# Kernel tuning notes

Measured on AMD Instinct MI355X. Metric: run time of the kernel, lower is better.

## Reference

```python
import jax, jax.numpy as jnp
import numpy as np

B, T = 64, 500
NUM_CONCEPT, DIM, SIZE_MEM = 1024, 64, 50


def setup_inputs() -> dict:
    key = jax.random.key(0)
    ks = jax.random.split(key, 16)
    d = DIM

    def lin(k, fin, fout):
        k1, k2 = jax.random.split(k)
        s = 1.0 / np.sqrt(fin)
        return (jax.random.uniform(k1, (fin, fout), jnp.float32, -s, s),
                jax.random.uniform(k2, (fout,), jnp.float32, -s, s))

    Wf, bf = lin(ks[4], 2 * d, d)
    We, be = lin(ks[5], d, d)
    Wa, ba = lin(ks[6], d, d)
    Wab, bab = lin(ks[7], d, 1)
    Wd, bd = lin(ks[8], d, 1)
    return {
        'concept_seq': jax.random.randint(ks[0], (B, T), 0, NUM_CONCEPT),
        'correct_seq': jax.random.randint(ks[1], (B, T), 0, 2),
        'num_concept': NUM_CONCEPT,
        'embed_key': jax.random.normal(ks[2], (NUM_CONCEPT, d), jnp.float32),
        'embed_value': jax.random.normal(ks[3], (2 * NUM_CONCEPT, d), jnp.float32),
        'Mk': jax.random.normal(ks[9], (SIZE_MEM, d), jnp.float32) * np.sqrt(2.0 / d),
        'Mv0': jax.random.normal(ks[10], (SIZE_MEM, d), jnp.float32) * np.sqrt(2.0 / d),
        'Wf': Wf, 'bf': bf, 'We': We, 'be': be, 'Wa': Wa, 'ba': ba,
        'Wab': Wab, 'bab': bab, 'Wd': Wd, 'bd': bd,
    }


def _forward(concept_seq, correct_seq, num_concept, embed_key, embed_value,
             Mk, Mv0, Wf, bf, We, be, Wa, ba, Wab, bab, Wd, bd):
    x = concept_seq + num_concept * correct_seq          # [B,T]
    k = embed_key[concept_seq]                           # [B,T,d]
    v = embed_value[x]                                   # [B,T,d]
    w = jax.nn.softmax(jnp.einsum('btd,sd->bts', k, Mk), axis=-1)  # [B,T,S]
    e = jax.nn.sigmoid(v @ We + be)                      # [B,T,d]
    a = jnp.tanh(v @ Wa + ba)                            # [B,T,d]

    bsz = concept_seq.shape[0]
    Mv_init = jnp.broadcast_to(Mv0, (bsz,) + Mv0.shape)  # [B,S,d]

    def step(Mvt, inp):
        wt, et, at = inp                                 # [B,S],[B,d],[B,d]
        u = wt[:, :, None]
        Mv_new = Mvt * (1.0 - u * et[:, None, :]) + u * at[:, None, :]
        return Mv_new, Mvt                               # emit pre-update state

    wT = jnp.swapaxes(w, 0, 1)                           # [T,B,S]
    eT = jnp.swapaxes(e, 0, 1)
    aT = jnp.swapaxes(a, 0, 1)
    _, Mv_pre = jax.lax.scan(step, Mv_init, (wT, eT, aT))  # [T,B,S,d]

    r = jnp.einsum('tbs,tbsd->btd', wT, Mv_pre)          # read content [B,T,d]
    f = jnp.tanh(jnp.concatenate([r, k], axis=-1) @ Wf + bf)
    stu_ability = jnp.tanh(f @ Wab + bab)                # [B,T,1] (dropout = eval identity)
    que_diff = jnp.tanh(k @ Wd + bd)                     # [B,T,1]
    return jax.nn.sigmoid(3.0 * stu_ability - que_diff)[..., 0]  # [B,T]


def reference(concept_seq, correct_seq, num_concept, embed_key, embed_value,
              Mk, Mv0, Wf, bf, We, be, Wa, ba, Wab, bab, Wd, bd):
    return _forward(concept_seq, correct_seq, num_concept, embed_key, embed_value,
                    Mk, Mv0, Wf, bf, We, be, Wa, ba, Wab, bab, Wd, bd)
```

## Files before the change

### kernel.cpp

```cpp
#include <hip/hip_runtime.h>
#include <hip/hip_bf16.h>
#include <math.h>

#define BB 64
#define TT 500
#define DD 64
#define SS 50
#define CH 20
#define NCH (TT / CH)

__device__ __forceinline__ float sigmoidf_(float x) { return 1.0f / (1.0f + __expf(-x)); }

__device__ __forceinline__ float rdlane(float v, int l) {
    return __int_as_float(__builtin_amdgcn_readlane(__float_as_int(v), l));
}

#define PIN() asm volatile("" ::: "memory")

__global__ __launch_bounds__(64) void k1_tables(
    const float* __restrict__ embed_key,
    const float* __restrict__ embed_value,
    const float* __restrict__ Mk,
    const float* __restrict__ We, const float* __restrict__ be,
    const float* __restrict__ Wa, const float* __restrict__ ba,
    int ncon, int nv,
    float* __restrict__ wTab, float* __restrict__ eaTab)
{
    const int lane = threadIdx.x;
    if ((int)blockIdx.x < ncon) {
        const int c = blockIdx.x;
        __shared__ float mkS[SS][DD + 1];
        __shared__ float kS[DD];
        kS[lane] = embed_key[c * DD + lane];
        for (int s = 0; s < SS; ++s)
            mkS[s][lane] = Mk[s * DD + lane];
        __syncthreads();

        float sc = -1e30f;
        if (lane < SS) {
            float acc = 0.f;
            #pragma unroll
            for (int dd = 0; dd < DD; ++dd)
                acc = fmaf(kS[dd], mkS[lane][dd], acc);
            sc = acc;
        }
        float m = sc;
        #pragma unroll
        for (int off = 32; off >= 1; off >>= 1)
            m = fmaxf(m, __shfl_xor(m, off));
        float ex = (lane < SS) ? __expf(sc - m) : 0.f;
        float ssum = ex;
        #pragma unroll
        for (int off = 32; off >= 1; off >>= 1)
            ssum += __shfl_xor(ssum, off);
        if (lane < SS)
            wTab[c * SS + lane] = ex / ssum;
    } else {
        const int x = blockIdx.x - ncon;
        __shared__ float vS[DD];
        vS[lane] = embed_value[x * DD + lane];
        __syncthreads();
        float acc_e = be[lane];
        float acc_a = ba[lane];
        #pragma unroll
        for (int i = 0; i < DD; ++i) {
            const float vi = vS[i];
            acc_e = fmaf(vi, We[i * DD + lane], acc_e);
            acc_a = fmaf(vi, Wa[i * DD + lane], acc_a);
        }
        float2 ea;
        ea.x = sigmoidf_(acc_e);
        ea.y = tanhf(acc_a);
        *(float2*)&eaTab[((size_t)x * DD + lane) * 2] = ea;
    }
}

#define GW(WD, KK, T0) {                                                     \
    const int idx_ = lane + 64 * (KK);                                       \
    const int tt_ = idx_ >> 4, j_ = idx_ & 15;                               \
    const int s_ = st + j_;                                                  \
    WD = (s_ < en) ? wTab[cL[(T0) + tt_] * SS + s_] : 0.f; }

#define GLOAD(P, T0)                                                         \
    GW(w##P##0, 0, T0) GW(w##P##1, 1, T0) GW(w##P##2, 2, T0)                 \
    GW(w##P##3, 3, T0) GW(w##P##4, 4, T0)                                    \
    _Pragma("unroll")                                                        \
    for (int tt = 0; tt < CH; ++tt) {                                        \
        const int xx_ = xL[(T0) + tt];                                       \
        ea##P[tt] = *(const float2*)&eaTab[((size_t)xx_ * DD + lane) * 2]; }

#define UPD(WW, JJ) {                                                        \
    const float mv_ = Mv[JJ];                                                \
    if ((JJ) & 1) r1 = fmaf(WW, mv_, r1); else r0 = fmaf(WW, mv_, r0);       \
    Mv[JJ] = fmaf(-(WW), fmaf(e_, mv_, -a_), mv_); }

#define STEP(P, WREG, tc, T0) {                                              \
    const float e_ = ea##P[tc].x, a_ = ea##P[tc].y;                          \
    const int qb_ = ((tc) & 3) * 16;                                         \
    const float x0_  = rdlane(WREG, qb_ + 0);                                \
    const float x1_  = rdlane(WREG, qb_ + 1);                                \
    const float x2_  = rdlane(WREG, qb_ + 2);                                \
    const float x3_  = rdlane(WREG, qb_ + 3);                                \
    const float x4_  = rdlane(WREG, qb_ + 4);                                \
    const float x5_  = rdlane(WREG, qb_ + 5);                                \
    const float x6_  = rdlane(WREG, qb_ + 6);                                \
    const float x7_  = rdlane(WREG, qb_ + 7);                                \
    const float x8_  = rdlane(WREG, qb_ + 8);                                \
    const float x9_  = rdlane(WREG, qb_ + 9);                                \
    const float x10_ = rdlane(WREG, qb_ + 10);                               \
    const float x11_ = rdlane(WREG, qb_ + 11);                               \
    const float x12_ = rdlane(WREG, qb_ + 12);                               \
    float r0 = 0.f, r1 = 0.f;                                                \
    UPD(x0_, 0)  UPD(x1_, 1)  UPD(x2_, 2)  UPD(x3_, 3)                       \
    UPD(x4_, 4)  UPD(x5_, 5)  UPD(x6_, 6)  UPD(x7_, 7)                       \
    UPD(x8_, 8)  UPD(x9_, 9)  UPD(x10_, 10) UPD(x11_, 11) UPD(x12_, 12)      \
    rp[(size_t)((T0) + (tc)) * DD] = r0 + r1; }

#define CCOMP(P, T0)                                                         \
    STEP(P, w##P##0, 0, T0)  STEP(P, w##P##0, 1, T0)                         \
    STEP(P, w##P##0, 2, T0)  STEP(P, w##P##0, 3, T0)                         \
    STEP(P, w##P##1, 4, T0)  STEP(P, w##P##1, 5, T0)                         \
    STEP(P, w##P##1, 6, T0)  STEP(P, w##P##1, 7, T0)                         \
    STEP(P, w##P##2, 8, T0)  STEP(P, w##P##2, 9, T0)                         \
    STEP(P, w##P##2, 10, T0) STEP(P, w##P##2, 11, T0)                        \
    STEP(P, w##P##3, 12, T0) STEP(P, w##P##3, 13, T0)                        \
    STEP(P, w##P##3, 14, T0) STEP(P, w##P##3, 15, T0)                        \
    STEP(P, w##P##4, 16, T0) STEP(P, w##P##4, 17, T0)                        \
    STEP(P, w##P##4, 18, T0) STEP(P, w##P##4, 19, T0)

__global__ __launch_bounds__(64, 1) void k2_scan(
    const int* __restrict__ cseq,
    const int* __restrict__ corr,
    const int* __restrict__ ncp,
    const float* __restrict__ wTab,
    const float* __restrict__ eaTab,
    const float* __restrict__ Mv0,
    float* __restrict__ rPart)
{
    const int b = blockIdx.x >> 2;
    const int sgB = blockIdx.x & 3;
    const int lane = threadIdx.x;
    const int nc = ncp[0];

    __shared__ int xL[TT];
    __shared__ int cL[TT];
    for (int i = lane; i < TT; i += 64) {
        const int c = cseq[b * TT + i];
        cL[i] = c;
        xL[i] = c + nc * corr[b * TT + i];
    }
    __syncthreads();

    const int st = (SS * sgB) >> 2;
    const int en = (SS * (sgB + 1)) >> 2;

    float Mv[13];
    #pragma unroll
    for (int j = 0; j < 13; ++j) {
        const int s = st + j;
        Mv[j] = (s < en) ? Mv0[s * DD + lane] : 0.f;
    }

    float* rp = rPart + ((size_t)sgB * BB + b) * TT * DD + lane;

    float2 eaA[CH], eaB[CH];
    float wA0, wA1, wA2, wA3, wA4, wB0, wB1, wB2, wB3, wB4;

    GLOAD(A, 0)
    PIN();

    for (int ch = 0; ch < NCH - 1; ch += 2) {
        const int T0a = ch * CH;
        const int T0b = T0a + CH;
        const int T0c = T0a + 2 * CH;
        GLOAD(B, T0b)
        PIN();
        CCOMP(A, T0a)
        GLOAD(A, T0c)
        PIN();
        CCOMP(B, T0b)
    }
    CCOMP(A, (NCH - 1) * CH)
}

__global__ __launch_bounds__(256) void k3_output(
    const int* __restrict__ cseq,
    const float* __restrict__ embed_key,
    const float* __restrict__ rPart,
    const float* __restrict__ Wf, const float* __restrict__ bf,
    const float* __restrict__ Wab, const float* __restrict__ bab,
    const float* __restrict__ Wd, const float* __restrict__ bd,
    float* __restrict__ out)
{
    const int tid = threadIdx.x;
    const int tx = tid & 15, ty = tid >> 4;
    const int bt0 = blockIdx.x * 64;

    __shared__ float __align__(16) wfS[128][64];
    __shared__ float __align__(16) catT[128][68];
    __shared__ float qS[64];
    __shared__ float redS[64][17];

    #pragma unroll
    for (int k = 0; k < 8; ++k) {
        const int idx = tid + k * 256;
        ((float4*)wfS)[idx] = ((const float4*)Wf)[idx];
    }

    {
        const int d = tid & 63;
        const int g = tid >> 6;
        const float wd = Wd[d];
        #pragma unroll
        for (int m = 0; m < 16; ++m) {
            const int btl = g + 4 * m;
            const int bt = bt0 + btl;
            const int c = cseq[bt];
            const size_t o = (size_t)bt * DD + d;
            const float r = rPart[o]
                          + rPart[(size_t)1 * BB * TT * DD + o]
                          + rPart[(size_t)2 * BB * TT * DD + o]
                          + rPart[(size_t)3 * BB * TT * DD + o];
            const float kv = embed_key[c * DD + d];
            catT[d][btl] = r;
            catT[64 + d][btl] = kv;
            float q = kv * wd;
            #pragma unroll
            for (int off = 32; off >= 1; off >>= 1)
                q += __shfl_xor(q, off);
            if (d == 0) qS[btl] = q;
        }
    }
    __syncthreads();

    float acc[4][4] = {{0.f}};
    #pragma unroll 8
    for (int i = 0; i < 128; ++i) {
        const float4 wf = *(const float4*)&wfS[i][tx * 4];
        const float4 ct = *(const float4*)&catT[i][ty * 4];
        acc[0][0] = fmaf(ct.x, wf.x, acc[0][0]);
        acc[0][1] = fmaf(ct.x, wf.y, acc[0][1]);
        acc[0][2] = fmaf(ct.x, wf.z, acc[0][2]);
        acc[0][3] = fmaf(ct.x, wf.w, acc[0][3]);
        acc[1][0] = fmaf(ct.y, wf.x, acc[1][0]);
        acc[1][1] = fmaf(ct.y, wf.y, acc[1][1]);
        acc[1][2] = fmaf(ct.y, wf.z, acc[1][2]);
        acc[1][3] = fmaf(ct.y, wf.w, acc[1][3]);
        acc[2][0] = fmaf(ct.z, wf.x, acc[2][0]);
        acc[2][1] = fmaf(ct.z, wf.y, acc[2][1]);
        acc[2][2] = fmaf(ct.z, wf.z, acc[2][2]);
        acc[2][3] = fmaf(ct.z, wf.w, acc[2][3]);
        acc[3][0] = fmaf(ct.w, wf.x, acc[3][0]);
        acc[3][1] = fmaf(ct.w, wf.y, acc[3][1]);
        acc[3][2] = fmaf(ct.w, wf.z, acc[3][2]);
        acc[3][3] = fmaf(ct.w, wf.w, acc[3][3]);
    }

    #pragma unroll
    for (int ii = 0; ii < 4; ++ii) {
        float p = 0.f;
        #pragma unroll
        for (int jj = 0; jj < 4; ++jj) {
            const int j = tx * 4 + jj;
            const float f = tanhf(acc[ii][jj] + bf[j]);
            p = fmaf(f, Wab[j], p);
        }
        redS[ty * 4 + ii][tx] = p;
    }
    __syncthreads();

    if (tid < 64) {
        const int btl = tid;
        float s = 0.f;
        #pragma unroll
        for (int t2 = 0; t2 < 16; ++t2)
            s += redS[btl][t2];
        const float stu  = tanhf(s + bab[0]);
        const float diff = tanhf(qS[btl] + bd[0]);
        out[bt0 + btl] = sigmoidf_(3.0f * stu - diff);
    }
}

extern "C" void kernel_launch(void* const* d_in, const int* in_sizes, int n_in,
                              void* d_out, int out_size, void* d_ws, size_t ws_size,
                              hipStream_t stream)
{
    const int*   concept_seq = (const int*)  d_in[0];
    const int*   correct_seq = (const int*)  d_in[1];
    const int*   num_concept = (const int*)  d_in[2];
    const float* embed_key   = (const float*)d_in[3];
    const float* embed_value = (const float*)d_in[4];
    const float* Mk          = (const float*)d_in[5];
    const float* Mv0         = (const float*)d_in[6];
    const float* Wf          = (const float*)d_in[7];
    const float* bf          = (const float*)d_in[8];
    const float* We          = (const float*)d_in[9];
    const float* be          = (const float*)d_in[10];
    const float* Wa          = (const float*)d_in[11];
    const float* ba          = (const float*)d_in[12];
    const float* Wab         = (const float*)d_in[13];
    const float* bab         = (const float*)d_in[14];
    const float* Wd          = (const float*)d_in[15];
    const float* bd          = (const float*)d_in[16];
    float* out = (float*)d_out;

    const int NCON = in_sizes[3] / DD;
    const int NV   = in_sizes[4] / DD;

    float* wTab  = (float*)d_ws;
    float* eaTab = wTab + (size_t)NCON * SS;
    float* rPart = eaTab + (size_t)NV * DD * 2;

    k1_tables<<<NCON + NV, 64, 0, stream>>>(
        embed_key, embed_value, Mk, We, be, Wa, ba,
        NCON, NV, wTab, eaTab);

    k2_scan<<<BB * 4, 64, 0, stream>>>(
        concept_seq, correct_seq, num_concept,
        wTab, eaTab, Mv0, rPart);

    k3_output<<<(BB * TT) / 64, 256, 0, stream>>>(
        concept_seq, embed_key, rPart,
        Wf, bf, Wab, bab, Wd, bd, out);
}
```

Before: 176.8 us.

## Split scan memory slots across 8 waves per batch and reduce reads in LDS

The scan kernel goes from 4 single-wave blocks per batch row (13 memory slots each) to one 512-thread block per batch row with 8 waves handling 6-7 slots each. Each 20-step chunk's partial read vectors are written to shared memory and summed in-block, so the four global partial buffers and their summation in the output kernel are removed. This shortens each wave's serial per-step chain and cuts global traffic. The cost is two block-wide barriers per chunk, which can stall waves, and only 64 blocks running on the GPU.

```diff
diff --git a/kernel.cpp b/kernel.cpp
--- a/kernel.cpp
+++ b/kernel.cpp
@@ -8,6 +8,7 @@
 #define SS 50
 #define CH 20
 #define NCH (TT / CH)
+#define NW 8
 
 __device__ __forceinline__ float sigmoidf_(float x) { return 1.0f / (1.0f + __expf(-x)); }
 
@@ -76,14 +77,13 @@
 }
 
 #define GW(WD, KK, T0) {                                                     \
-    const int idx_ = lane + 64 * (KK);                                       \
-    const int tt_ = idx_ >> 4, j_ = idx_ & 15;                               \
+    const int tt_ = (KK) * 8 + (lane >> 3);                                  \
+    const int j_ = lane & 7;                                                 \
     const int s_ = st + j_;                                                  \
-    WD = (s_ < en) ? wTab[cL[(T0) + tt_] * SS + s_] : 0.f; }
+    WD = (tt_ < CH && s_ < en) ? wTab[cL[(T0) + tt_] * SS + s_] : 0.f; }
 
 #define GLOAD(P, T0)                                                         \
     GW(w##P##0, 0, T0) GW(w##P##1, 1, T0) GW(w##P##2, 2, T0)                 \
-    GW(w##P##3, 3, T0) GW(w##P##4, 4, T0)                                    \
     _Pragma("unroll")                                                        \
     for (int tt = 0; tt < CH; ++tt) {                                        \
         const int xx_ = xL[(T0) + tt];                                       \
@@ -94,77 +94,81 @@
     if ((JJ) & 1) r1 = fmaf(WW, mv_, r1); else r0 = fmaf(WW, mv_, r0);       \
     Mv[JJ] = fmaf(-(WW), fmaf(e_, mv_, -a_), mv_); }
 
-#define STEP(P, WREG, tc, T0) {                                              \
+#define STEP(P, WREG, tc) {                                                  \
     const float e_ = ea##P[tc].x, a_ = ea##P[tc].y;                          \
-    const int qb_ = ((tc) & 3) * 16;                                         \
-    const float x0_  = rdlane(WREG, qb_ + 0);                                \
-    const float x1_  = rdlane(WREG, qb_ + 1);                                \
-    const float x2_  = rdlane(WREG, qb_ + 2);                                \
-    const float x3_  = rdlane(WREG, qb_ + 3);                                \
-    const float x4_  = rdlane(WREG, qb_ + 4);                                \
-    const float x5_  = rdlane(WREG, qb_ + 5);                                \
-    const float x6_  = rdlane(WREG, qb_ + 6);                                \
-    const float x7_  = rdlane(WREG, qb_ + 7);                                \
-    const float x8_  = rdlane(WREG, qb_ + 8);                                \
-    const float x9_  = rdlane(WREG, qb_ + 9);                                \
-    const float x10_ = rdlane(WREG, qb_ + 10);                               \
-    const float x11_ = rdlane(WREG, qb_ + 11);                               \
-    const float x12_ = rdlane(WREG, qb_ + 12);                               \
+    const float x0_ = rdlane(WREG, ((tc) & 7) * 8 + 0);                      \
+    const float x1_ = rdlane(WREG, ((tc) & 7) * 8 + 1);                      \
+    const float x2_ = rdlane(WREG, ((tc) & 7) * 8 + 2);                      \
+    const float x3_ = rdlane(WREG, ((tc) & 7) * 8 + 3);                      \
+    const float x4_ = rdlane(WREG, ((tc) & 7) * 8 + 4);                      \
+    const float x5_ = rdlane(WREG, ((tc) & 7) * 8 + 5);                      \
+    const float x6_ = rdlane(WREG, ((tc) & 7) * 8 + 6);                      \
     float r0 = 0.f, r1 = 0.f;                                                \
-    UPD(x0_, 0)  UPD(x1_, 1)  UPD(x2_, 2)  UPD(x3_, 3)                       \
-    UPD(x4_, 4)  UPD(x5_, 5)  UPD(x6_, 6)  UPD(x7_, 7)                       \
-    UPD(x8_, 8)  UPD(x9_, 9)  UPD(x10_, 10) UPD(x11_, 11) UPD(x12_, 12)      \
-    rp[(size_t)((T0) + (tc)) * DD] = r0 + r1; }
-
-#define CCOMP(P, T0)                                                         \
-    STEP(P, w##P##0, 0, T0)  STEP(P, w##P##0, 1, T0)                         \
-    STEP(P, w##P##0, 2, T0)  STEP(P, w##P##0, 3, T0)                         \
-    STEP(P, w##P##1, 4, T0)  STEP(P, w##P##1, 5, T0)                         \
-    STEP(P, w##P##1, 6, T0)  STEP(P, w##P##1, 7, T0)                         \
-    STEP(P, w##P##2, 8, T0)  STEP(P, w##P##2, 9, T0)                         \
-    STEP(P, w##P##2, 10, T0) STEP(P, w##P##2, 11, T0)                        \
-    STEP(P, w##P##3, 12, T0) STEP(P, w##P##3, 13, T0)                        \
-    STEP(P, w##P##3, 14, T0) STEP(P, w##P##3, 15, T0)                        \
-    STEP(P, w##P##4, 16, T0) STEP(P, w##P##4, 17, T0)                        \
-    STEP(P, w##P##4, 18, T0) STEP(P, w##P##4, 19, T0)
-
-__global__ __launch_bounds__(64, 1) void k2_scan(
+    UPD(x0_, 0) UPD(x1_, 1) UPD(x2_, 2) UPD(x3_, 3)                          \
+    UPD(x4_, 4) UPD(x5_, 5) UPD(x6_, 6)                                      \
+    parts[tc][sg][lane] = r0 + r1; }
+
+#define CCOMP(P)                                                             \
+    STEP(P, w##P##0, 0)  STEP(P, w##P##0, 1)  STEP(P, w##P##0, 2)            \
+    STEP(P, w##P##0, 3)  STEP(P, w##P##0, 4)  STEP(P, w##P##0, 5)            \
+    STEP(P, w##P##0, 6)  STEP(P, w##P##0, 7)                                 \
+    STEP(P, w##P##1, 8)  STEP(P, w##P##1, 9)  STEP(P, w##P##1, 10)           \
+    STEP(P, w##P##1, 11) STEP(P, w##P##1, 12) STEP(P, w##P##1, 13)           \
+    STEP(P, w##P##1, 14) STEP(P, w##P##1, 15)                                \
+    STEP(P, w##P##2, 16) STEP(P, w##P##2, 17) STEP(P, w##P##2, 18)           \
+    STEP(P, w##P##2, 19)
+
+#define RED(T0) {                                                            \
+    __syncthreads();                                                         \
+    _Pragma("unroll")                                                        \
+    for (int o = tid; o < CH * DD; o += 512) {                               \
+        const int tc2 = o >> 6, d2 = o & 63;                                 \
+        float s_ = parts[tc2][0][d2] + parts[tc2][1][d2]                     \
+                 + parts[tc2][2][d2] + parts[tc2][3][d2]                     \
+                 + parts[tc2][4][d2] + parts[tc2][5][d2]                     \
+                 + parts[tc2][6][d2] + parts[tc2][7][d2];                    \
+        rOut[((size_t)b * TT + (T0) + tc2) * DD + d2] = s_;                  \
+    }                                                                        \
+    __syncthreads(); }
+
+__global__ __launch_bounds__(512) void k2_scan(
     const int* __restrict__ cseq,
     const int* __restrict__ corr,
     const int* __restrict__ ncp,
     const float* __restrict__ wTab,
     const float* __restrict__ eaTab,
     const float* __restrict__ Mv0,
-    float* __restrict__ rPart)
+    float* __restrict__ rOut)
 {
-    const int b = blockIdx.x >> 2;
-    const int sgB = blockIdx.x & 3;
-    const int lane = threadIdx.x;
+    const int b = blockIdx.x;
+    const int tid = threadIdx.x;
+    const int lane = tid & 63;
+    const int sg = tid >> 6;
     const int nc = ncp[0];
 
     __shared__ int xL[TT];
     __shared__ int cL[TT];
-    for (int i = lane; i < TT; i += 64) {
+    __shared__ float parts[CH][NW][DD];
+
+    for (int i = tid; i < TT; i += 512) {
         const int c = cseq[b * TT + i];
         cL[i] = c;
         xL[i] = c + nc * corr[b * TT + i];
     }
     __syncthreads();
 
-    const int st = (SS * sgB) >> 2;
-    const int en = (SS * (sgB + 1)) >> 2;
-
-    float Mv[13];
+    const int st = (sg < 2) ? sg * 7 : 14 + (sg - 2) * 6;
+    const int en = st + ((sg < 2) ? 7 : 6);
+
+    float Mv[7];
     #pragma unroll
-    for (int j = 0; j < 13; ++j) {
+    for (int j = 0; j < 7; ++j) {
         const int s = st + j;
         Mv[j] = (s < en) ? Mv0[s * DD + lane] : 0.f;
     }
 
-    float* rp = rPart + ((size_t)sgB * BB + b) * TT * DD + lane;
-
     float2 eaA[CH], eaB[CH];
-    float wA0, wA1, wA2, wA3, wA4, wB0, wB1, wB2, wB3, wB4;
+    float wA0, wA1, wA2, wB0, wB1, wB2;
 
     GLOAD(A, 0)
     PIN();
@@ -175,18 +179,21 @@
         const int T0c = T0a + 2 * CH;
         GLOAD(B, T0b)
         PIN();
-        CCOMP(A, T0a)
+        CCOMP(A)
+        RED(T0a)
         GLOAD(A, T0c)
         PIN();
-        CCOMP(B, T0b)
-    }
-    CCOMP(A, (NCH - 1) * CH)
+        CCOMP(B)
+        RED(T0b)
+    }
+    CCOMP(A)
+    RED((NCH - 1) * CH)
 }
 
 __global__ __launch_bounds__(256) void k3_output(
     const int* __restrict__ cseq,
     const float* __restrict__ embed_key,
-    const float* __restrict__ rPart,
+    const float* __restrict__ rOut,
     const float* __restrict__ Wf, const float* __restrict__ bf,
     const float* __restrict__ Wab, const float* __restrict__ bab,
     const float* __restrict__ Wd, const float* __restrict__ bd,
@@ -216,11 +223,7 @@
             const int btl = g + 4 * m;
             const int bt = bt0 + btl;
             const int c = cseq[bt];
-            const size_t o = (size_t)bt * DD + d;
-            const float r = rPart[o]
-                          + rPart[(size_t)1 * BB * TT * DD + o]
-                          + rPart[(size_t)2 * BB * TT * DD + o]
-                          + rPart[(size_t)3 * BB * TT * DD + o];
+            const float r  = rOut[(size_t)bt * DD + d];
             const float kv = embed_key[c * DD + d];
             catT[d][btl] = r;
             catT[64 + d][btl] = kv;
@@ -309,17 +312,17 @@
 
     float* wTab  = (float*)d_ws;
     float* eaTab = wTab + (size_t)NCON * SS;
-    float* rPart = eaTab + (size_t)NV * DD * 2;
+    float* rOut  = eaTab + (size_t)NV * DD * 2;
 
     k1_tables<<<NCON + NV, 64, 0, stream>>>(
         embed_key, embed_value, Mk, We, be, Wa, ba,
         NCON, NV, wTab, eaTab);
 
-    k2_scan<<<BB * 4, 64, 0, stream>>>(
+    k2_scan<<<BB, 512, 0, stream>>>(
         concept_seq, correct_seq, num_concept,
-        wTab, eaTab, Mv0, rPart);
+        wTab, eaTab, Mv0, rOut);
 
     k3_output<<<(BB * TT) / 64, 256, 0, stream>>>(
-        concept_seq, embed_key, rPart,
+        concept_seq, embed_key, rOut,
         Wf, bf, Wab, bab, Wd, bd, out);
 }
```

Result: slower. 189.7 us (+7.3%).

## Stage scan chunks through LDS double buffer and use packed FMA updates

Applied to the files above, without the earlier changes.

The recurrent scan kernel no longer keeps two register-resident chunks and broadcasts weights with readlane. It now issues global loads for the next chunk into registers, computes the current chunk from an LDS double buffer, and writes the staged data to LDS afterward. The memory update uses packed two-wide FMAs over pairs of slots. The output kernel replaces the per-row wavefront shuffle reduction for que_diff with a single-thread dot product over shared memory. This aims to cut readlane/VGPR pressure and halve FMA issue count, at the cost of LDS reads per step and a missing barrier, which is acceptable only because the block is a single wave.

```diff
diff --git a/kernel.cpp b/kernel.cpp
--- a/kernel.cpp
+++ b/kernel.cpp
@@ -9,11 +9,9 @@
 #define CH 20
 #define NCH (TT / CH)
 
+typedef float v2f __attribute__((ext_vector_type(2)));
+
 __device__ __forceinline__ float sigmoidf_(float x) { return 1.0f / (1.0f + __expf(-x)); }
-
-__device__ __forceinline__ float rdlane(float v, int l) {
-    return __int_as_float(__builtin_amdgcn_readlane(__float_as_int(v), l));
-}
 
 #define PIN() asm volatile("" ::: "memory")
 
@@ -75,58 +73,36 @@
     }
 }
 
-#define GW(WD, KK, T0) {                                                     \
-    const int idx_ = lane + 64 * (KK);                                       \
-    const int tt_ = idx_ >> 4, j_ = idx_ & 15;                               \
-    const int s_ = st + j_;                                                  \
-    WD = (s_ < en) ? wTab[cL[(T0) + tt_] * SS + s_] : 0.f; }
-
-#define GLOAD(P, T0)                                                         \
-    GW(w##P##0, 0, T0) GW(w##P##1, 1, T0) GW(w##P##2, 2, T0)                 \
-    GW(w##P##3, 3, T0) GW(w##P##4, 4, T0)                                    \
+#define STAGE_ISSUE(T0) {                                                    \
+    _Pragma("unroll")                                                        \
+    for (int kk = 0; kk < 5; ++kk) {                                         \
+        const int idx_ = lane + 64 * kk;                                     \
+        const int tt_ = idx_ >> 4, j_ = idx_ & 15;                           \
+        const int s_ = st + j_;                                              \
+        wr[kk] = (s_ < en) ? wTab[cL[(T0) + tt_] * SS + s_] : 0.f;           \
+    }                                                                        \
     _Pragma("unroll")                                                        \
     for (int tt = 0; tt < CH; ++tt) {                                        \
         const int xx_ = xL[(T0) + tt];                                       \
-        ea##P[tt] = *(const float2*)&eaTab[((size_t)xx_ * DD + lane) * 2]; }
-
-#define UPD(WW, JJ) {                                                        \
-    const float mv_ = Mv[JJ];                                                \
-    if ((JJ) & 1) r1 = fmaf(WW, mv_, r1); else r0 = fmaf(WW, mv_, r0);       \
-    Mv[JJ] = fmaf(-(WW), fmaf(e_, mv_, -a_), mv_); }
-
-#define STEP(P, WREG, tc, T0) {                                              \
-    const float e_ = ea##P[tc].x, a_ = ea##P[tc].y;                          \
-    const int qb_ = ((tc) & 3) * 16;                                         \
-    const float x0_  = rdlane(WREG, qb_ + 0);                                \
-    const float x1_  = rdlane(WREG, qb_ + 1);                                \
-    const float x2_  = rdlane(WREG, qb_ + 2);                                \
-    const float x3_  = rdlane(WREG, qb_ + 3);                                \
-    const float x4_  = rdlane(WREG, qb_ + 4);                                \
-    const float x5_  = rdlane(WREG, qb_ + 5);                                \
-    const float x6_  = rdlane(WREG, qb_ + 6);                                \
-    const float x7_  = rdlane(WREG, qb_ + 7);                                \
-    const float x8_  = rdlane(WREG, qb_ + 8);                                \
-    const float x9_  = rdlane(WREG, qb_ + 9);                                \
-    const float x10_ = rdlane(WREG, qb_ + 10);                               \
-    const float x11_ = rdlane(WREG, qb_ + 11);                               \
-    const float x12_ = rdlane(WREG, qb_ + 12);                               \
-    float r0 = 0.f, r1 = 0.f;                                                \
-    UPD(x0_, 0)  UPD(x1_, 1)  UPD(x2_, 2)  UPD(x3_, 3)                       \
-    UPD(x4_, 4)  UPD(x5_, 5)  UPD(x6_, 6)  UPD(x7_, 7)                       \
-    UPD(x8_, 8)  UPD(x9_, 9)  UPD(x10_, 10) UPD(x11_, 11) UPD(x12_, 12)      \
-    rp[(size_t)((T0) + (tc)) * DD] = r0 + r1; }
-
-#define CCOMP(P, T0)                                                         \
-    STEP(P, w##P##0, 0, T0)  STEP(P, w##P##0, 1, T0)                         \
-    STEP(P, w##P##0, 2, T0)  STEP(P, w##P##0, 3, T0)                         \
-    STEP(P, w##P##1, 4, T0)  STEP(P, w##P##1, 5, T0)                         \
-    STEP(P, w##P##1, 6, T0)  STEP(P, w##P##1, 7, T0)                         \
-    STEP(P, w##P##2, 8, T0)  STEP(P, w##P##2, 9, T0)                         \
-    STEP(P, w##P##2, 10, T0) STEP(P, w##P##2, 11, T0)                        \
-    STEP(P, w##P##3, 12, T0) STEP(P, w##P##3, 13, T0)                        \
-    STEP(P, w##P##3, 14, T0) STEP(P, w##P##3, 15, T0)                        \
-    STEP(P, w##P##4, 16, T0) STEP(P, w##P##4, 17, T0)                        \
-    STEP(P, w##P##4, 18, T0) STEP(P, w##P##4, 19, T0)
+        ear[tt] = *(const float2*)&eaTab[((size_t)xx_ * DD + lane) * 2];     \
+    } }
+
+#define STAGE_WRITE(BUF) {                                                   \
+    _Pragma("unroll")                                                        \
+    for (int kk = 0; kk < 5; ++kk) {                                         \
+        const int idx_ = lane + 64 * kk;                                     \
+        wL[BUF][idx_ >> 4][idx_ & 15] = wr[kk];                              \
+    }                                                                        \
+    _Pragma("unroll")                                                        \
+    for (int tt = 0; tt < CH; ++tt)                                          \
+        eaL[BUF][tt][lane] = ear[tt];                                        \
+    }
+
+#define PKSTEP(W2, JJ) {                                                     \
+    const v2f mv_ = Mv2[JJ];                                                 \
+    r2 = __builtin_elementwise_fma(W2, mv_, r2);                             \
+    const v2f g_ = __builtin_elementwise_fma(e2, mv_, na2);                  \
+    Mv2[JJ] = __builtin_elementwise_fma(-(W2), g_, mv_); }
 
 __global__ __launch_bounds__(64, 1) void k2_scan(
     const int* __restrict__ cseq,
@@ -144,6 +120,9 @@
 
     __shared__ int xL[TT];
     __shared__ int cL[TT];
+    __shared__ float __align__(16) wL[2][CH][16];
+    __shared__ float2 __align__(8) eaL[2][CH][DD];
+
     for (int i = lane; i < TT; i += 64) {
         const int c = cseq[b * TT + i];
         cL[i] = c;
@@ -154,33 +133,54 @@
     const int st = (SS * sgB) >> 2;
     const int en = (SS * (sgB + 1)) >> 2;
 
-    float Mv[13];
+    v2f Mv2[7];
     #pragma unroll
-    for (int j = 0; j < 13; ++j) {
-        const int s = st + j;
-        Mv[j] = (s < en) ? Mv0[s * DD + lane] : 0.f;
+    for (int jj = 0; jj < 7; ++jj) {
+        const int s0 = st + 2 * jj, s1 = s0 + 1;
+        v2f m;
+        m.x = (s0 < en) ? Mv0[s0 * DD + lane] : 0.f;
+        m.y = (s1 < en) ? Mv0[s1 * DD + lane] : 0.f;
+        Mv2[jj] = m;
     }
 
     float* rp = rPart + ((size_t)sgB * BB + b) * TT * DD + lane;
 
-    float2 eaA[CH], eaB[CH];
-    float wA0, wA1, wA2, wA3, wA4, wB0, wB1, wB2, wB3, wB4;
-
-    GLOAD(A, 0)
-    PIN();
-
-    for (int ch = 0; ch < NCH - 1; ch += 2) {
-        const int T0a = ch * CH;
-        const int T0b = T0a + CH;
-        const int T0c = T0a + 2 * CH;
-        GLOAD(B, T0b)
-        PIN();
-        CCOMP(A, T0a)
-        GLOAD(A, T0c)
-        PIN();
-        CCOMP(B, T0b)
-    }
-    CCOMP(A, (NCH - 1) * CH)
+    float wr[5];
+    float2 ear[CH];
+
+    STAGE_ISSUE(0)
+    STAGE_WRITE(0)
+
+    for (int ch = 0; ch < NCH; ++ch) {
+        const int buf = ch & 1;
+        if (ch + 1 < NCH) {
+            STAGE_ISSUE((ch + 1) * CH)
+            PIN();
+        }
+        const int T0 = ch * CH;
+        #pragma unroll
+        for (int tc = 0; tc < CH; ++tc) {
+            const float4 wq0 = *(const float4*)&wL[buf][tc][0];
+            const float4 wq1 = *(const float4*)&wL[buf][tc][4];
+            const float4 wq2 = *(const float4*)&wL[buf][tc][8];
+            const v2f   w6_ = *(const v2f*)  &wL[buf][tc][12];
+            const float2 ea = eaL[buf][tc][lane];
+            const v2f e2  = {ea.x, ea.x};
+            const v2f na2 = {-ea.y, -ea.y};
+            const v2f w0_ = {wq0.x, wq0.y};
+            const v2f w1_ = {wq0.z, wq0.w};
+            const v2f w2_ = {wq1.x, wq1.y};
+            const v2f w3_ = {wq1.z, wq1.w};
+            const v2f w4_ = {wq2.x, wq2.y};
+            const v2f w5_ = {wq2.z, wq2.w};
+            v2f r2 = {0.f, 0.f};
+            PKSTEP(w0_, 0) PKSTEP(w1_, 1) PKSTEP(w2_, 2) PKSTEP(w3_, 3)
+            PKSTEP(w4_, 4) PKSTEP(w5_, 5) PKSTEP(w6_, 6)
+            rp[(size_t)(T0 + tc) * DD] = r2.x + r2.y;
+        }
+        if (ch + 1 < NCH)
+            STAGE_WRITE((ch + 1) & 1)
+    }
 }
 
 __global__ __launch_bounds__(256) void k3_output(
@@ -199,6 +199,7 @@
     __shared__ float __align__(16) wfS[128][64];
     __shared__ float __align__(16) catT[128][68];
     __shared__ float qS[64];
+    __shared__ float wdS[64];
     __shared__ float redS[64][17];
 
     #pragma unroll
@@ -206,11 +207,11 @@
         const int idx = tid + k * 256;
         ((float4*)wfS)[idx] = ((const float4*)Wf)[idx];
     }
+    if (tid < 64) wdS[tid] = Wd[tid];
 
     {
         const int d = tid & 63;
         const int g = tid >> 6;
-        const float wd = Wd[d];
         #pragma unroll
         for (int m = 0; m < 16; ++m) {
             const int btl = g + 4 * m;
@@ -221,17 +222,20 @@
                           + rPart[(size_t)1 * BB * TT * DD + o]
                           + rPart[(size_t)2 * BB * TT * DD + o]
                           + rPart[(size_t)3 * BB * TT * DD + o];
-            const float kv = embed_key[c * DD + d];
             catT[d][btl] = r;
-            catT[64 + d][btl] = kv;
-            float q = kv * wd;
-            #pragma unroll
-            for (int off = 32; off >= 1; off >>= 1)
-                q += __shfl_xor(q, off);
-            if (d == 0) qS[btl] = q;
+            catT[64 + d][btl] = embed_key[c * DD + d];
         }
     }
     __syncthreads();
+
+    if (tid < 64) {
+        const int btl = tid;
+        float q = 0.f;
+        #pragma unroll
+        for (int i = 0; i < DD; ++i)
+            q = fmaf(catT[64 + i][btl], wdS[i], q);
+        qS[btl] = q;
+    }
 
     float acc[4][4] = {{0.f}};
     #pragma unroll 8
```

Result: faster. 170.7 us (-3.5%).
